# Kernel tuning notes

Hardware: AMD Instinct MI355X
Metric: run time of the kernel (lower is better)

## Reference

```python
import jax, jax.numpy as jnp
import numpy as np

BS, N, D = 8, 2048, 512


def setup_inputs() -> dict:
    key = jax.random.key(0)
    ks = jax.random.split(key, 8)
    s = 0.05  # small scale keeps exp(k + bias) numerically tame
    inp = jax.random.normal(ks[0], (BS, N, D), dtype=jnp.float32)
    Wq = jax.random.normal(ks[1], (D, D), dtype=jnp.float32) * s
    bq = jax.random.normal(ks[2], (D,), dtype=jnp.float32) * s
    Wk = jax.random.normal(ks[3], (D, D), dtype=jnp.float32) * s
    bk = jax.random.normal(ks[4], (D,), dtype=jnp.float32) * s
    Wv = jax.random.normal(ks[5], (D, D), dtype=jnp.float32) * s
    bv = jax.random.normal(ks[6], (D,), dtype=jnp.float32) * s
    pos_bias = jax.random.normal(ks[7], (N, N), dtype=jnp.float32) * s
    return {"input": inp, "Wq": Wq, "bq": bq, "Wk": Wk, "bk": bk,
            "Wv": Wv, "bv": bv, "pos_bias": pos_bias}


def reference(input, Wq, bq, Wk, bk, Wv, bv, pos_bias):
    # q, k, v projections: (bs, n, d)
    q = input @ Wq + bq
    k = input @ Wk + bk
    v = input @ Wv + bv
    # AFT-Full: out[b,i,d] = sigmoid(q)[b,i,d] *
    #   sum_j exp(k[b,j,d] + B[i,j]) * v[b,j,d] / sum_j exp(k[b,j,d] + B[i,j])
    # Factor exp(k + B) = exp(B) * exp(k): avoids the (n,bs,n,d) broadcast,
    # identical math to the torch source.
    ek = jnp.exp(k)                       # (bs, n, d)
    eB = jnp.exp(pos_bias)                # (n, n), rows = query pos i
    numerator = jnp.einsum('ij,bjd->bid', eB, ek * v)
    denominator = jnp.einsum('ij,bjd->bid', eB, ek)
    return jax.nn.sigmoid(q) * (numerator / denominator)
```

## Files before the change

kernel.cpp:

```cpp
#include <hip/hip_runtime.h>
#include <stdint.h>

#define N_SEQ 2048
#define D_MODEL 512
#define MROWS 16384
#define NT_K 32

typedef __attribute__((ext_vector_type(8))) short bf16x8;
typedef __attribute__((ext_vector_type(4))) float f32x4;

__device__ __forceinline__ short f2bf(float f) {
  union { float f; uint32_t u; } x; x.f = f;
  uint32_t r = x.u + 0x7FFFu + ((x.u >> 16) & 1u);
  return (short)(uint16_t)(r >> 16);
}
__device__ __forceinline__ unsigned short f2h(float f) {
  union { _Float16 h; unsigned short u; } x; x.h = (_Float16)f; return x.u;
}
__device__ __forceinline__ float h2f(unsigned short u) {
  union { unsigned short u; _Float16 h; } x; x.u = u; return (float)x.h;
}

__device__ __forceinline__ void gload_lds16(const void* g, void* l) {
  __builtin_amdgcn_global_load_lds(
      (__attribute__((address_space(1))) void*)(void*)g,
      (__attribute__((address_space(3))) void*)l, 16, 0, 0);
}


__global__ void k_conv_bf16(const float* __restrict__ in,
                            short* __restrict__ a, int n4) {
  int stride = gridDim.x * blockDim.x;
  for (int i = blockIdx.x * blockDim.x + threadIdx.x; i < n4; i += stride) {
    float4 v = reinterpret_cast<const float4*>(in)[i];
    short4 h;
    h.x = f2bf(v.x); h.y = f2bf(v.y); h.z = f2bf(v.z); h.w = f2bf(v.w);
    reinterpret_cast<short4*>(a)[i] = h;
  }
}

__global__ void k_prep_eb(const float* __restrict__ pb, short* __restrict__ eb,
                          int n4) {
  int stride = gridDim.x * blockDim.x;
  for (int i = blockIdx.x * blockDim.x + threadIdx.x; i < n4; i += stride) {
    float4 v = reinterpret_cast<const float4*>(pb)[i];
    short4 o;
    o.x = f2bf(expf(v.x));
    o.y = f2bf(expf(v.y));
    o.z = f2bf(expf(v.z));
    o.w = f2bf(expf(v.w));
    reinterpret_cast<short4*>(eb)[i] = o;
  }
}

__global__ void k_prep_w(const float* __restrict__ Wq, const float* __restrict__ Wk,
                         const float* __restrict__ Wv, short* __restrict__ wh) {
  int t = blockIdx.x * blockDim.x + threadIdx.x;
  if (t >= 1536 * 512) return;
  int c = t >> 9, k = t & 511;
  float v;
  if (c < 512) v = Wq[k * 512 + c];
  else {
    int cc = c - 512, d = cc >> 1;
    v = (cc & 1) ? Wv[k * 512 + d] : Wk[k * 512 + d];
  }
  wh[t] = f2bf(v);
}

__global__ __launch_bounds__(256) void k_proj(
    const short* __restrict__ A, const short* __restrict__ W,
    const float* __restrict__ bq, const float* __restrict__ bk,
    const float* __restrict__ bv,
    unsigned short* __restrict__ sigq, short* __restrict__ Xf) {
  __shared__ short lA[128 * 64], lB[128 * 64];
  const int tid = threadIdx.x;
  const int lane = tid & 63, wid = tid >> 6;
  const int wr = wid >> 1, wc = wid & 1;
  const int lrow = lane & 15;
  const int kq = (lane >> 4) << 4;
  const int row0 = blockIdx.x * 128;
  const int col0 = blockIdx.y * 128;

  const f32x4 fzero = {0.f, 0.f, 0.f, 0.f};
  f32x4 acc[4][4];
#pragma unroll
  for (int m = 0; m < 4; ++m)
#pragma unroll
    for (int n = 0; n < 4; ++n) acc[m][n] = fzero;

  const short* gA = A + row0 * 512;
  const short* gB = W + col0 * 512;

  for (int kt = 0; kt < 8; ++kt) {
    const int kb = kt * 64;
#pragma unroll
    for (int p = 0; p < 4; ++p) {
      int c = p * 256 + tid;
      int B = c << 4;
      int r = B >> 7;
      int wp = (B & 127) ^ ((r & 7) << 4);
      int ke = wp >> 1;
      int goff = r * 512 + kb + ke;
      int loff = (p * 256 + wid * 64) << 3;
      gload_lds16(gA + goff, lA + loff);
      gload_lds16(gB + goff, lB + loff);
    }
    __syncthreads();
#pragma unroll
    for (int ks = 0; ks < 2; ++ks) {
      int kb2 = kq + ks * 64;
      bf16x8 fb[4];
#pragma unroll
      for (int n = 0; n < 4; ++n) {
        int r = wc * 64 + n * 16 + lrow;
        fb[n] = *(const bf16x8*)((const char*)lB + (r << 7) +
                                 (kb2 ^ ((r & 7) << 4)));
      }
#pragma unroll
      for (int m = 0; m < 4; ++m) {
        int r = wr * 64 + m * 16 + lrow;
        bf16x8 fa = *(const bf16x8*)((const char*)lA + (r << 7) +
                                     (kb2 ^ ((r & 7) << 4)));
#pragma unroll
        for (int n = 0; n < 4; ++n)
          acc[m][n] = __builtin_amdgcn_mfma_f32_16x16x32_bf16(fa, fb[n], acc[m][n], 0, 0, 0);
      }
    }
    __syncthreads();
  }

  const int rbase = row0 + wr * 64 + ((lane >> 4) << 2);
  if (col0 < 512) {
#pragma unroll
    for (int n = 0; n < 4; ++n) {
      int c = col0 + wc * 64 + n * 16 + lrow;
      float bias = bq[c];
#pragma unroll
      for (int m = 0; m < 4; ++m) {
        int gr = rbase + m * 16;
#pragma unroll
        for (int r = 0; r < 4; ++r) {
          float q = acc[m][n][r] + bias;
          sigq[(gr + r) * 512 + c] = f2h(1.f / (1.f + expf(-q)));
        }
      }
    }
  } else {
    int s = lane & 1;
#pragma unroll
    for (int n = 0; n < 4; ++n) {
      int c = col0 + wc * 64 + n * 16 + lrow;
      int d = (c - 512) >> 1;
      float bias = s ? bv[d] : bk[d];
#pragma unroll
      for (int m = 0; m < 4; ++m) {
        int gr = rbase + m * 16;
        int b = gr >> 11;
        int j = gr & 2047;
        f32x4 val;
#pragma unroll
        for (int r = 0; r < 4; ++r) val[r] = acc[m][n][r] + bias;
        if (!s) {
#pragma unroll
          for (int r = 0; r < 4; ++r) val[r] = expf(val[r]);
        }
        f32x4 oth;
#pragma unroll
        for (int r = 0; r < 4; ++r) oth[r] = __shfl_xor(val[r], 1);
        if (!s) {
          short4 wq, eq;
          wq.x = f2bf(val[0] * oth[0]); eq.x = f2bf(val[0]);
          wq.y = f2bf(val[1] * oth[1]); eq.y = f2bf(val[1]);
          wq.z = f2bf(val[2] * oth[2]); eq.z = f2bf(val[2]);
          wq.w = f2bf(val[3] * oth[3]); eq.w = f2bf(val[3]);
          int colp = b * 1024 + 2 * d;
          int kg = j >> 5;
          int sub = ((j >> 3) & 3) << 4;
          int e0 = j & 4;
          int ctn = colp >> 4;
          int lnn = (colp & 15) | sub;
          int lnd = ((colp + 1) & 15) | sub;
          *(short4*)&Xf[(kg << 18) + (ctn << 9) + (lnn << 3) + e0] = wq;
          *(short4*)&Xf[(kg << 18) + (ctn << 9) + (lnd << 3) + e0] = eq;
        }
      }
    }
  }
}

__global__ __launch_bounds__(512, 4) void k_main7(
    const short* __restrict__ eB, const short* __restrict__ Xf,
    const unsigned short* __restrict__ sigq, float* __restrict__ out) {
  extern __shared__ short lds[];
  const int tid = threadIdx.x;
  const int lane = tid & 63, wid = tid >> 6;
  const int wr = wid >> 1, wc = wid & 1;
  const int lrow = lane & 15;
  const int khi = (lane >> 4) << 4;

  const int bid = blockIdx.x;
  const int xcd = bid & 7, bj = bid >> 3;
  const int row0 = (bj & 7) * 256;
  const int col0 = ((xcd << 3) + (bj >> 3)) * 128;

  const f32x4 fzero = {0.f, 0.f, 0.f, 0.f};
  f32x4 acc[4][4];
#pragma unroll
  for (int m = 0; m < 4; ++m)
#pragma unroll
    for (int n = 0; n < 4; ++n) acc[m][n] = fzero;

  const short* gA = eB + row0 * 2048;
  const int pfo = (col0 << 5) + (wc << 11) + (lane << 3);

  auto STAGE = [&](int kt) {
    const short* src = gA + kt * 64;
    const int sb = (kt & 1) << 14;
#pragma unroll
    for (int p = 0; p < 4; ++p) {
      int c = p * 512 + tid;
      int r = c >> 3;
      int ke = ((((c & 7) << 4) ^ ((r & 7) << 4)) >> 1);
      gload_lds16(src + r * 2048 + ke,
                  lds + sb + ((p * 512 + wid * 64) << 3));
    }
  };
  auto LDA = [&](int b, int ks, int m) -> bf16x8 {
    int R = wr * 64 + m * 16 + lrow;
    int kb = ks * 64 + khi;
    return *(const bf16x8*)((const char*)lds + (b << 15) + R * 128 +
                            (kb ^ ((R & 7) << 4)));
  };
  auto LOADFB = [&](bf16x8* fb, int kt, int ks) {
    const short* base = Xf + (((size_t)(kt * 2 + ks)) << 18) + pfo;
#pragma unroll
    for (int n = 0; n < 4; ++n)
      fb[n] = *(const bf16x8*)(base + (n << 9));
  };

  bf16x8 fb[8];

  STAGE(0);
  LOADFB(fb, 0, 0);
  LOADFB(fb + 4, 0, 1);
  __syncthreads();

  for (int t = 0; t < NT_K; ++t) {
    const int b = t & 1;
    if (t + 1 < NT_K) STAGE(t + 1);
    {
      bf16x8 fa[4];
#pragma unroll
      for (int m = 0; m < 4; ++m) fa[m] = LDA(b, 0, m);
      __builtin_amdgcn_s_setprio(1);
#pragma unroll
      for (int m = 0; m < 4; ++m)
#pragma unroll
        for (int n = 0; n < 4; ++n)
          acc[m][n] = __builtin_amdgcn_mfma_f32_16x16x32_bf16(
              fa[m], fb[n], acc[m][n], 0, 0, 0);
      __builtin_amdgcn_s_setprio(0);
    }
    if (t + 1 < NT_K) LOADFB(fb, t + 1, 0);
    {
      bf16x8 fa[4];
#pragma unroll
      for (int m = 0; m < 4; ++m) fa[m] = LDA(b, 1, m);
      __builtin_amdgcn_s_setprio(1);
#pragma unroll
      for (int m = 0; m < 4; ++m)
#pragma unroll
        for (int n = 0; n < 4; ++n)
          acc[m][n] = __builtin_amdgcn_mfma_f32_16x16x32_bf16(
              fa[m], fb[4 + n], acc[m][n], 0, 0, 0);
      __builtin_amdgcn_s_setprio(0);
    }
    if (t + 1 < NT_K) LOADFB(fb + 4, t + 1, 1);
    __syncthreads();
  }

  const int rbase = row0 + wr * 64 + ((lane >> 4) << 2);
#pragma unroll
  for (int n = 0; n < 4; ++n) {
    int c = col0 + wc * 64 + n * 16 + lrow;
    int b = c >> 10;
    int d = (c & 1023) >> 1;
#pragma unroll
    for (int m = 0; m < 4; ++m) {
      f32x4 den;
#pragma unroll
      for (int r = 0; r < 4; ++r) den[r] = __shfl_xor(acc[m][n][r], 1);
      if ((lane & 1) == 0) {
#pragma unroll
        for (int r = 0; r < 4; ++r) {
          int i2 = rbase + m * 16 + r;
          int idx = (b * 2048 + i2) * 512 + d;
          out[idx] = h2f(sigq[idx]) * (acc[m][n][r] / den[r]);
        }
      }
    }
  }
}

extern "C" void kernel_launch(void* const* d_in, const int* in_sizes, int n_in,
                              void* d_out, int out_size, void* d_ws, size_t ws_size,
                              hipStream_t stream) {
  const float* in = (const float*)d_in[0];
  const float* Wq = (const float*)d_in[1];
  const float* bq = (const float*)d_in[2];
  const float* Wk = (const float*)d_in[3];
  const float* bk = (const float*)d_in[4];
  const float* Wv = (const float*)d_in[5];
  const float* bv = (const float*)d_in[6];
  const float* pb = (const float*)d_in[7];
  float* out = (float*)d_out;

  char* ws = (char*)d_ws;
  short* Xf = (short*)ws;
  short* eB = (short*)(ws + 33554432);
  short* Ah = (short*)(ws + 41943040);
  short* Wh = (short*)(ws + 58720256);
  unsigned short* sigq = (unsigned short*)(ws + 60293120);

  (void)hipFuncSetAttribute((const void*)k_main7,
                            hipFuncAttributeMaxDynamicSharedMemorySize, 65536);

  k_conv_bf16<<<2048, 256, 0, stream>>>(in, Ah, MROWS * D_MODEL / 4);
  k_prep_w<<<3072, 256, 0, stream>>>(Wq, Wk, Wv, Wh);
  k_prep_eb<<<2048, 256, 0, stream>>>(pb, eB, N_SEQ * N_SEQ / 4);

  dim3 gp(128, 12);
  k_proj<<<gp, 256, 0, stream>>>(Ah, Wh, bq, bk, bv, sigq, Xf);

  k_main7<<<dim3(512), 512, 65536, stream>>>(eB, Xf, sigq, out);
}
```

Baseline: 149.1 us.

## Switch main AFT GEMM to 32x32x16 MFMA tiles with matching Xf layout

Replaces the 16x16x32 bf16 MFMA tiling in the main eB x [ek*v, ek] GEMM with 32x32x16 MFMAs over 2x2 accumulator blocks per wave. The projection kernel now writes Xf in the fragment layout the 32x32 instruction expects, and the LDS A-fragment reads and epilogue row mapping are updated to match. The larger MFMA shape issues fewer instructions and needs fewer fragment loads per flop, in exchange for 16-wide accumulator vectors and a more scattered epilogue store pattern.

```diff
diff --git a/kernel.cpp b/kernel.cpp
--- a/kernel.cpp
+++ b/kernel.cpp
@@ -8,6 +8,7 @@
 
 typedef __attribute__((ext_vector_type(8))) short bf16x8;
 typedef __attribute__((ext_vector_type(4))) float f32x4;
+typedef __attribute__((ext_vector_type(16))) float f32x16;
 
 __device__ __forceinline__ short f2bf(float f) {
   union { float f; uint32_t u; } x; x.f = f;
@@ -174,44 +175,43 @@
           wq.z = f2bf(val[2] * oth[2]); eq.z = f2bf(val[2]);
           wq.w = f2bf(val[3] * oth[3]); eq.w = f2bf(val[3]);
           int colp = b * 1024 + 2 * d;
-          int kg = j >> 5;
-          int sub = ((j >> 3) & 3) << 4;
-          int e0 = j & 4;
-          int ctn = colp >> 4;
-          int lnn = (colp & 15) | sub;
-          int lnd = ((colp + 1) & 15) | sub;
-          *(short4*)&Xf[(kg << 18) + (ctn << 9) + (lnn << 3) + e0] = wq;
-          *(short4*)&Xf[(kg << 18) + (ctn << 9) + (lnd << 3) + e0] = eq;
+          int kg16 = j >> 4;
+          int lnn = (colp & 31) + (((j >> 3) & 1) << 5);
+          int e0 = j & 7;
+          size_t base = ((size_t)kg16 << 17) + (((size_t)(colp >> 5)) << 9);
+          *(short4*)&Xf[base + (lnn << 3) + e0] = wq;
+          *(short4*)&Xf[base + ((lnn + 1) << 3) + e0] = eq;
         }
       }
     }
   }
 }
 
-__global__ __launch_bounds__(512, 4) void k_main7(
+__global__ __launch_bounds__(512, 4) void k_main8(
     const short* __restrict__ eB, const short* __restrict__ Xf,
     const unsigned short* __restrict__ sigq, float* __restrict__ out) {
   extern __shared__ short lds[];
   const int tid = threadIdx.x;
   const int lane = tid & 63, wid = tid >> 6;
   const int wr = wid >> 1, wc = wid & 1;
-  const int lrow = lane & 15;
-  const int khi = (lane >> 4) << 4;
+  const int l31 = lane & 31;
+  const int lhi = lane >> 5;
 
   const int bid = blockIdx.x;
   const int xcd = bid & 7, bj = bid >> 3;
   const int row0 = (bj & 7) * 256;
   const int col0 = ((xcd << 3) + (bj >> 3)) * 128;
 
-  const f32x4 fzero = {0.f, 0.f, 0.f, 0.f};
-  f32x4 acc[4][4];
-#pragma unroll
-  for (int m = 0; m < 4; ++m)
-#pragma unroll
-    for (int n = 0; n < 4; ++n) acc[m][n] = fzero;
+  f32x16 acc[2][2];
+#pragma unroll
+  for (int m = 0; m < 2; ++m)
+#pragma unroll
+    for (int n = 0; n < 2; ++n)
+#pragma unroll
+      for (int r = 0; r < 16; ++r) acc[m][n][r] = 0.f;
 
   const short* gA = eB + row0 * 2048;
-  const int pfo = (col0 << 5) + (wc << 11) + (lane << 3);
+  const int pfo = ((col0 >> 5) + wc * 2) * 512 + (lane << 3);
 
   auto STAGE = [&](int kt) {
     const short* src = gA + kt * 64;
@@ -220,22 +220,24 @@
     for (int p = 0; p < 4; ++p) {
       int c = p * 512 + tid;
       int r = c >> 3;
-      int ke = ((((c & 7) << 4) ^ ((r & 7) << 4)) >> 1);
+      int ke = ((((c & 7) << 4) ^ (((c >> 3) & 7) << 4)) >> 1);
       gload_lds16(src + r * 2048 + ke,
                   lds + sb + ((p * 512 + wid * 64) << 3));
     }
   };
   auto LDA = [&](int b, int ks, int m) -> bf16x8 {
-    int R = wr * 64 + m * 16 + lrow;
-    int kb = ks * 64 + khi;
+    int R = wr * 64 + m * 32 + l31;
+    int kb = ks * 32 + (lhi << 4);
     return *(const bf16x8*)((const char*)lds + (b << 15) + R * 128 +
                             (kb ^ ((R & 7) << 4)));
   };
-  auto LOADFB = [&](bf16x8* fb, int kt, int ks) {
-    const short* base = Xf + (((size_t)(kt * 2 + ks)) << 18) + pfo;
-#pragma unroll
-    for (int n = 0; n < 4; ++n)
-      fb[n] = *(const bf16x8*)(base + (n << 9));
+  auto LOADFB = [&](bf16x8* fb, int kt, int h) {
+#pragma unroll
+    for (int k2 = 0; k2 < 2; ++k2) {
+      const short* base = Xf + (((size_t)(kt * 4 + h * 2 + k2)) << 17) + pfo;
+      fb[k2 * 2 + 0] = *(const bf16x8*)(base);
+      fb[k2 * 2 + 1] = *(const bf16x8*)(base + 512);
+    }
   };
 
   bf16x8 fb[8];
@@ -251,49 +253,57 @@
     {
       bf16x8 fa[4];
 #pragma unroll
-      for (int m = 0; m < 4; ++m) fa[m] = LDA(b, 0, m);
+      for (int k2 = 0; k2 < 2; ++k2)
+#pragma unroll
+        for (int m = 0; m < 2; ++m) fa[k2 * 2 + m] = LDA(b, k2, m);
       __builtin_amdgcn_s_setprio(1);
 #pragma unroll
-      for (int m = 0; m < 4; ++m)
-#pragma unroll
-        for (int n = 0; n < 4; ++n)
-          acc[m][n] = __builtin_amdgcn_mfma_f32_16x16x32_bf16(
-              fa[m], fb[n], acc[m][n], 0, 0, 0);
+      for (int k2 = 0; k2 < 2; ++k2)
+#pragma unroll
+        for (int m = 0; m < 2; ++m)
+#pragma unroll
+          for (int n = 0; n < 2; ++n)
+            acc[m][n] = __builtin_amdgcn_mfma_f32_32x32x16_bf16(
+                fa[k2 * 2 + m], fb[k2 * 2 + n], acc[m][n], 0, 0, 0);
       __builtin_amdgcn_s_setprio(0);
     }
     if (t + 1 < NT_K) LOADFB(fb, t + 1, 0);
     {
       bf16x8 fa[4];
 #pragma unroll
-      for (int m = 0; m < 4; ++m) fa[m] = LDA(b, 1, m);
+      for (int k2 = 0; k2 < 2; ++k2)
+#pragma unroll
+        for (int m = 0; m < 2; ++m) fa[k2 * 2 + m] = LDA(b, 2 + k2, m);
       __builtin_amdgcn_s_setprio(1);
 #pragma unroll
-      for (int m = 0; m < 4; ++m)
-#pragma unroll
-        for (int n = 0; n < 4; ++n)
-          acc[m][n] = __builtin_amdgcn_mfma_f32_16x16x32_bf16(
-              fa[m], fb[4 + n], acc[m][n], 0, 0, 0);
+      for (int k2 = 0; k2 < 2; ++k2)
+#pragma unroll
+        for (int m = 0; m < 2; ++m)
+#pragma unroll
+          for (int n = 0; n < 2; ++n)
+            acc[m][n] = __builtin_amdgcn_mfma_f32_32x32x16_bf16(
+                fa[k2 * 2 + m], fb[4 + k2 * 2 + n], acc[m][n], 0, 0, 0);
       __builtin_amdgcn_s_setprio(0);
     }
     if (t + 1 < NT_K) LOADFB(fb + 4, t + 1, 1);
     __syncthreads();
   }
 
-  const int rbase = row0 + wr * 64 + ((lane >> 4) << 2);
-#pragma unroll
-  for (int n = 0; n < 4; ++n) {
-    int c = col0 + wc * 64 + n * 16 + lrow;
+  const int rb32 = row0 + wr * 64 + (lhi << 2);
+#pragma unroll
+  for (int n = 0; n < 2; ++n) {
+    int c = col0 + wc * 64 + n * 32 + l31;
     int b = c >> 10;
     int d = (c & 1023) >> 1;
 #pragma unroll
-    for (int m = 0; m < 4; ++m) {
-      f32x4 den;
-#pragma unroll
-      for (int r = 0; r < 4; ++r) den[r] = __shfl_xor(acc[m][n][r], 1);
+    for (int m = 0; m < 2; ++m) {
+      f32x16 den;
+#pragma unroll
+      for (int r = 0; r < 16; ++r) den[r] = __shfl_xor(acc[m][n][r], 1);
       if ((lane & 1) == 0) {
 #pragma unroll
-        for (int r = 0; r < 4; ++r) {
-          int i2 = rbase + m * 16 + r;
+        for (int r = 0; r < 16; ++r) {
+          int i2 = rb32 + m * 32 + (r & 3) + ((r >> 2) << 3);
           int idx = (b * 2048 + i2) * 512 + d;
           out[idx] = h2f(sigq[idx]) * (acc[m][n][r] / den[r]);
         }
@@ -322,7 +332,7 @@
   short* Wh = (short*)(ws + 58720256);
   unsigned short* sigq = (unsigned short*)(ws + 60293120);
 
-  (void)hipFuncSetAttribute((const void*)k_main7,
+  (void)hipFuncSetAttribute((const void*)k_main8,
                             hipFuncAttributeMaxDynamicSharedMemorySize, 65536);
 
   k_conv_bf16<<<2048, 256, 0, stream>>>(in, Ah, MROWS * D_MODEL / 4);
@@ -332,5 +342,5 @@
   dim3 gp(128, 12);
   k_proj<<<gp, 256, 0, stream>>>(Ah, Wh, bq, bk, bv, sigq, Xf);
 
-  k_main7<<<dim3(512), 512, 65536, stream>>>(eB, Xf, sigq, out);
-}
+  k_main8<<<dim3(512), 512, 65536, stream>>>(eB, Xf, sigq, out);
+}
```

Result: slower. 165.8 us (+11.2%).
